# Kernel optimization log

Hardware: AMD Instinct MI355X
Metric: run time of the kernel (lower is better)

## Reference

```python
import jax, jax.numpy as jnp
import numpy as np

B, S, D, H = 2, 2048, 1024, 16
HD = D // H  # head_dim = 64


def setup_inputs() -> dict:
    key = jax.random.key(0)
    ks = jax.random.split(key, 11)
    sc = 1.0 / np.sqrt(D)
    inp = {
        "query": jax.random.normal(ks[0], (B, S, D), jnp.float32),
        "key_": jax.random.normal(ks[1], (B, S, D), jnp.float32),
        "value": jax.random.normal(ks[2], (B, S, D), jnp.float32),
        "Wq": jax.random.normal(ks[3], (D, D), jnp.float32) * sc,
        "bq": jnp.zeros((D,), jnp.float32),
        "Wk": jax.random.normal(ks[4], (D, D), jnp.float32) * sc,
        "bk": jnp.zeros((D,), jnp.float32),
        "Wv": jax.random.normal(ks[5], (D, D), jnp.float32) * sc,
        "bv": jnp.zeros((D,), jnp.float32),
        "Wo": jax.random.normal(ks[6], (D, D), jnp.float32) * sc,
        "bo": jnp.zeros((D,), jnp.float32),
    }
    return inp


def _split_heads(x):
    # [B,S,D] -> [B,H,S,HD]
    return x.reshape(B, -1, H, HD).transpose(0, 2, 1, 3)


def reference(query, key_, value, Wq, bq, Wk, bk, Wv, bv, Wo, bo):
    q = _split_heads(query @ Wq.T + bq)
    k = _split_heads(key_ @ Wk.T + bk)
    v = _split_heads(value @ Wv.T + bv)
    scores = jnp.einsum("bhqd,bhkd->bhqk", q, k) / jnp.sqrt(jnp.float32(HD))
    attn = jax.nn.softmax(scores, axis=-1)  # dropout is identity in eval
    out = jnp.einsum("bhqk,bhkd->bhqd", attn, v)
    out = out.transpose(0, 2, 1, 3).reshape(B, -1, D)
    return out @ Wo.T + bo
```

## Files before the change

kernel.cpp:

```cpp
#include <hip/hip_runtime.h>
#include <hip/hip_bf16.h>
#include <stdint.h>

#define B_  2
#define S_  2048
#define D_  1024
#define H_  16
#define HD_ 64
#define M_  (B_*S_)

typedef __bf16 bf16x8 __attribute__((ext_vector_type(8)));
typedef float  f32x4  __attribute__((ext_vector_type(4)));
typedef unsigned int u32x4 __attribute__((ext_vector_type(4)));
typedef unsigned int u32x2 __attribute__((ext_vector_type(2)));
typedef unsigned short ushort_t;
typedef ushort_t u16x8 __attribute__((ext_vector_type(8)));

#define LOG2E 1.44269504088896f

#if __has_builtin(__builtin_amdgcn_exp2f)
#define EXP2(x) __builtin_amdgcn_exp2f(x)
#else
#define EXP2(x) exp2f(x)
#endif

__device__ __forceinline__ ushort_t f2bf(float f) {
    return __builtin_bit_cast(ushort_t, (__bf16)f);
}
__device__ __forceinline__ bf16x8 load_frag(const ushort_t* p) {
    u32x4 r = *reinterpret_cast<const u32x4*>(p);
    return __builtin_bit_cast(bf16x8, r);
}
__device__ __forceinline__ bf16x8 lds_frag(const ushort_t* p) {
    u32x4 r = *reinterpret_cast<const u32x4*>(p);
    return __builtin_bit_cast(bf16x8, r);
}
__device__ __forceinline__ void gld_lds16(const ushort_t* g, ushort_t* l) {
    __builtin_amdgcn_global_load_lds(
        (const __attribute__((address_space(1))) void*)g,
        (__attribute__((address_space(3))) void*)l, 16, 0, 0);
}

__device__ __forceinline__ void cvt_body(const float* __restrict__ in,
                                         ushort_t* __restrict__ out, int i) {
    f32x4 v0 = *reinterpret_cast<const f32x4*>(in + i);
    f32x4 v1 = *reinterpret_cast<const f32x4*>(in + i + 4);
    u16x8 o;
#pragma unroll
    for (int j = 0; j < 4; ++j) { o[j] = f2bf(v0[j]); o[4 + j] = f2bf(v1[j]); }
    *reinterpret_cast<u16x8*>(out + i) = o;
}

__global__ __launch_bounds__(256) void cvt_all_kernel(
    const float* q, const float* k, const float* v,
    const float* fwq, const float* fwk, const float* fwv, const float* fwo,
    ushort_t* oq, ushort_t* ok, ushort_t* ov,
    ushort_t* owq, ushort_t* owk, ushort_t* owv, ushort_t* owo)
{
    const size_t T = (size_t)M_ * D_;
    const size_t U = (size_t)D_ * D_;
    const size_t idx = ((size_t)blockIdx.x * 256 + threadIdx.x) * 8;
    const float* in; ushort_t* out; size_t off;
    if (idx < 3 * T) {
        const size_t w = idx >> 22; off = idx & (T - 1);
        in  = (w == 0) ? q  : (w == 1) ? k  : v;
        out = (w == 0) ? oq : (w == 1) ? ok : ov;
    } else {
        const size_t r = idx - 3 * T;
        const size_t w = r >> 20; off = r & (U - 1);
        in  = (w == 0) ? fwq : (w == 1) ? fwk : (w == 2) ? fwv : fwo;
        out = (w == 0) ? owq : (w == 1) ? owk : (w == 2) ? owv : owo;
    }
    cvt_body(in, out, (int)off);
}

__device__ __forceinline__ void gemm_body(const ushort_t* __restrict__ X,
                                          const ushort_t* __restrict__ W,
                                          const float* __restrict__ bias,
                                          void* __restrict__ out, int mode)
{
    __shared__ ushort_t lA[3][128 * 32];
    __shared__ ushort_t lB[3][128 * 32];

    const int tid  = threadIdx.x;
    const int lane = tid & 63;
    const int wv   = tid >> 6;
    const int m0   = blockIdx.x * 128;
    const int n0   = blockIdx.y * 128;
    const int wr   = (wv >> 1) * 64;
    const int wc   = (wv & 1) * 64;
    const int l15  = lane & 15;
    const int lg   = lane >> 4;

    f32x4 acc[4][4];
#pragma unroll
    for (int i = 0; i < 4; ++i)
#pragma unroll
        for (int j = 0; j < 4; ++j) acc[i][j] = (f32x4){0.f, 0.f, 0.f, 0.f};

    const int srow = lane >> 2;
    const int sk   = (lane & 3) * 8;
    const int c0   = wv * 2, c1 = wv * 2 + 1;
    const size_t arow0 = (size_t)(m0 + c0 * 16 + srow) * D_ + sk;
    const size_t arow1 = (size_t)(m0 + c1 * 16 + srow) * D_ + sk;
    const size_t brow0 = (size_t)(n0 + c0 * 16 + srow) * D_ + sk;
    const size_t brow1 = (size_t)(n0 + c1 * 16 + srow) * D_ + sk;

    auto stage = [&](int ktile, int bufi) {
        const int k0 = ktile * 32;
        gld_lds16(X + arow0 + k0, &lA[bufi][c0 * 512]);
        gld_lds16(X + arow1 + k0, &lA[bufi][c1 * 512]);
        gld_lds16(W + brow0 + k0, &lB[bufi][c0 * 512]);
        gld_lds16(W + brow1 + k0, &lB[bufi][c1 * 512]);
    };

    const int NKT = D_ / 32;
    stage(0, 0);
    stage(1, 1);

    int cur = 0;
    for (int kt = 0; kt < NKT; ++kt) {
        __builtin_amdgcn_s_barrier();
        if (kt + 2 < NKT) {
            int nxt = cur + 2; if (nxt >= 3) nxt -= 3;
            stage(kt + 2, nxt);
            asm volatile("s_waitcnt vmcnt(8)" ::: "memory");
        } else if (kt + 2 == NKT) {
            asm volatile("s_waitcnt vmcnt(4)" ::: "memory");
        } else {
            asm volatile("s_waitcnt vmcnt(0)" ::: "memory");
        }
        __builtin_amdgcn_s_barrier();
        __builtin_amdgcn_sched_barrier(0);

        bf16x8 a[4], b[4];
#pragma unroll
        for (int i = 0; i < 4; ++i)
            a[i] = lds_frag(&lA[cur][(wr + i * 16 + l15) * 32 + lg * 8]);
#pragma unroll
        for (int j = 0; j < 4; ++j)
            b[j] = lds_frag(&lB[cur][(wc + j * 16 + l15) * 32 + lg * 8]);
#pragma unroll
        for (int i = 0; i < 4; ++i)
#pragma unroll
            for (int j = 0; j < 4; ++j)
                acc[i][j] = __builtin_amdgcn_mfma_f32_16x16x32_bf16(a[i], b[j], acc[i][j], 0, 0, 0);

        cur = (cur == 2) ? 0 : cur + 1;
    }

#pragma unroll
    for (int i = 0; i < 4; ++i) {
#pragma unroll
        for (int j = 0; j < 4; ++j) {
            const int gcol = n0 + wc + j * 16 + l15;
            const float bv = bias[gcol];
#pragma unroll
            for (int r = 0; r < 4; ++r) {
                const int grow = m0 + wr + i * 16 + lg * 4 + r;
                float v = acc[i][j][r] + bv;
                if (mode == 0) v *= 0.125f * LOG2E;
                if (mode == 3) {
                    ((float*)out)[(size_t)grow * D_ + gcol] = v;
                } else {
                    const int b = grow >> 11, s = grow & (S_ - 1);
                    const int h = gcol >> 6,  hd = gcol & 63;
                    size_t addr;
                    if (mode == 2) addr = ((size_t)(b * H_ + h) * HD_ + hd) * S_ + s;
                    else           addr = ((size_t)(b * H_ + h) * S_ + s) * HD_ + hd;
                    ((ushort_t*)out)[addr] = f2bf(v);
                }
            }
        }
    }
}

__global__ __launch_bounds__(256) void qkv_kernel(
    const ushort_t* q_in, const ushort_t* k_in, const ushort_t* v_in,
    const ushort_t* Wq, const ushort_t* Wk, const ushort_t* Wv,
    const float* bq, const float* bk, const float* bv,
    ushort_t* qo, ushort_t* ko, ushort_t* vo)
{
    const int z = blockIdx.z;
    const ushort_t* X  = (z == 0) ? q_in : (z == 1) ? k_in : v_in;
    const ushort_t* W  = (z == 0) ? Wq   : (z == 1) ? Wk   : Wv;
    const float*    bs = (z == 0) ? bq   : (z == 1) ? bk   : bv;
    ushort_t*       o  = (z == 0) ? qo   : (z == 1) ? ko   : vo;
    gemm_body(X, W, bs, o, (z == 2) ? 2 : z);
}

__global__ __launch_bounds__(256) void oproj_kernel(
    const ushort_t* X, const ushort_t* W, const float* bias, float* out)
{
    gemm_body(X, W, bias, out, 3);
}

#define PST2 40
#define KVB 64
#define NT  (S_ / KVB)
#define SM_K0 0
#define SM_K1 4096
#define SM_V0 8192
#define SM_V1 12288
#define SM_P  16384
#define SM_TOT (16384 + 8 * 32 * PST2)

__global__ __launch_bounds__(512, 4) void attn_kernel(
    const ushort_t* __restrict__ Q, const ushort_t* __restrict__ K,
    const ushort_t* __restrict__ VT, ushort_t* __restrict__ O)
{
    __shared__ ushort_t smem[SM_TOT];

    const int lane = threadIdx.x & 63;
    const int wv   = threadIdx.x >> 6;
    const int wq   = wv & 3;
    const int wkv  = wv >> 2;
    const int bh   = blockIdx.x;
    const int qb   = blockIdx.y;
    const int qbase = qb * 128 + wq * 32;
    const int l15  = lane & 15;
    const int lg   = lane >> 4;

    const ushort_t* Qp = Q  + (size_t)bh * S_ * HD_;
    const ushort_t* Kp = K  + (size_t)bh * S_ * HD_;
    const ushort_t* Vp = VT + (size_t)bh * HD_ * S_;

    const int kr = threadIdx.x >> 3;
    const int kc = ((threadIdx.x & 7) ^ (kr & 7)) * 8;
    const int koff = threadIdx.x * 8;

    auto stage = [&](int tile, ushort_t* kdst, ushort_t* vdst) {
        gld_lds16(Kp + (size_t)(tile * KVB + kr) * HD_ + kc, kdst + koff);
        gld_lds16(Vp + (size_t)kr * S_ + tile * KVB + kc,    vdst + koff);
    };

    int offk[2][2];
#pragma unroll
    for (int j = 0; j < 2; ++j)
#pragma unroll
        for (int c = 0; c < 2; ++c)
            offk[j][c] = (wkv * 32 + j * 16 + l15) * 64 +
                         ((c * 32 + lg * 8) ^ ((l15 & 7) << 3));
    int offv[4];
#pragma unroll
    for (int dt = 0; dt < 4; ++dt)
        offv[dt] = (dt * 16 + l15) * 64 +
                   ((wkv * 32 + lg * 8) ^ ((l15 & 7) << 3));

    bf16x8 aq[2][2];
#pragma unroll
    for (int qh = 0; qh < 2; ++qh)
#pragma unroll
        for (int c = 0; c < 2; ++c)
            aq[c][qh] = load_frag(Qp + (size_t)(qbase + qh * 16 + l15) * HD_ + c * 32 + lg * 8);

    f32x4 accO[4][2];
#pragma unroll
    for (int dt = 0; dt < 4; ++dt)
#pragma unroll
        for (int qh = 0; qh < 2; ++qh) accO[dt][qh] = (f32x4){0.f, 0.f, 0.f, 0.f};
    float lrun0 = 0.f, lrun1 = 0.f;

    ushort_t* pbuf = &smem[SM_P + wv * 32 * PST2];

    stage(0, &smem[SM_K0], &smem[SM_V0]);

    for (int t = 0; t < NT; ++t) {
        const int cur = t & 1;
        const ushort_t* kb = cur ? &smem[SM_K1] : &smem[SM_K0];
        const ushort_t* vb = cur ? &smem[SM_V1] : &smem[SM_V0];

        __builtin_amdgcn_s_barrier();
        if (t + 1 < NT) {
            stage(t + 1, cur ? &smem[SM_K0] : &smem[SM_K1],
                          cur ? &smem[SM_V0] : &smem[SM_V1]);
            asm volatile("s_waitcnt vmcnt(2)" ::: "memory");
        } else {
            asm volatile("s_waitcnt vmcnt(0)" ::: "memory");
        }
        __builtin_amdgcn_s_barrier();
        __builtin_amdgcn_sched_barrier(0);

        f32x4 st[2][2];
#pragma unroll
        for (int j = 0; j < 2; ++j)
#pragma unroll
            for (int qh = 0; qh < 2; ++qh) st[j][qh] = (f32x4){0.f, 0.f, 0.f, 0.f};
        __builtin_amdgcn_s_setprio(1);
#pragma unroll
        for (int j = 0; j < 2; ++j) {
            bf16x8 k0 = lds_frag(&kb[offk[j][0]]);
            bf16x8 k1 = lds_frag(&kb[offk[j][1]]);
            st[j][0] = __builtin_amdgcn_mfma_f32_16x16x32_bf16(k0, aq[0][0], st[j][0], 0, 0, 0);
            st[j][0] = __builtin_amdgcn_mfma_f32_16x16x32_bf16(k1, aq[1][0], st[j][0], 0, 0, 0);
            st[j][1] = __builtin_amdgcn_mfma_f32_16x16x32_bf16(k0, aq[0][1], st[j][1], 0, 0, 0);
            st[j][1] = __builtin_amdgcn_mfma_f32_16x16x32_bf16(k1, aq[1][1], st[j][1], 0, 0, 0);
        }
        __builtin_amdgcn_s_setprio(0);

#pragma unroll
        for (int qh = 0; qh < 2; ++qh) {
            float p[2][4];
#pragma unroll
            for (int j = 0; j < 2; ++j)
#pragma unroll
                for (int r = 0; r < 4; ++r)
                    p[j][r] = EXP2(st[j][qh][r]);
#pragma unroll
            for (int j = 0; j < 2; ++j) {
                u32x2 w;
                w[0] = (unsigned)f2bf(p[j][0]) | ((unsigned)f2bf(p[j][1]) << 16);
                w[1] = (unsigned)f2bf(p[j][2]) | ((unsigned)f2bf(p[j][3]) << 16);
                *reinterpret_cast<u32x2*>(
                    &pbuf[(qh * 16 + l15) * PST2 + j * 16 + lg * 4]) = w;
            }
            float s0 = (p[0][0] + p[0][1]) + (p[0][2] + p[0][3]);
            float s1 = (p[1][0] + p[1][1]) + (p[1][2] + p[1][3]);
            if (qh == 0) lrun0 += s0 + s1;
            else         lrun1 += s0 + s1;
        }

        bf16x8 ap[2];
#pragma unroll
        for (int qh = 0; qh < 2; ++qh)
            ap[qh] = lds_frag(&pbuf[(qh * 16 + l15) * PST2 + lg * 8]);

        __builtin_amdgcn_s_setprio(1);
#pragma unroll
        for (int dt = 0; dt < 4; ++dt) {
            bf16x8 vf = lds_frag(&vb[offv[dt]]);
            accO[dt][0] = __builtin_amdgcn_mfma_f32_16x16x32_bf16(vf, ap[0], accO[dt][0], 0, 0, 0);
            accO[dt][1] = __builtin_amdgcn_mfma_f32_16x16x32_bf16(vf, ap[1], accO[dt][1], 0, 0, 0);
        }
        __builtin_amdgcn_s_setprio(0);
    }

    lrun0 += __shfl_xor(lrun0, 16);
    lrun0 += __shfl_xor(lrun0, 32);
    lrun1 += __shfl_xor(lrun1, 16);
    lrun1 += __shfl_xor(lrun1, 32);

    __syncthreads();
    float* cbuf = (float*)smem;

    if (wkv == 1) {
#pragma unroll
        for (int qh = 0; qh < 2; ++qh) {
            const int rowq = (wq * 2 + qh) * 16 + l15;
#pragma unroll
            for (int dt = 0; dt < 4; ++dt)
                *reinterpret_cast<f32x4*>(&cbuf[rowq * 68 + dt * 16 + lg * 4]) = accO[dt][qh];
        }
        if (lane < 16) {
            cbuf[128 * 68 + (wq * 2 + 0) * 16 + lane] = lrun0;
            cbuf[128 * 68 + (wq * 2 + 1) * 16 + lane] = lrun1;
        }
    }
    __syncthreads();

    if (wkv == 0) {
        const int b = bh >> 4, h = bh & 15;
#pragma unroll
        for (int qh = 0; qh < 2; ++qh) {
            const int rowq = (wq * 2 + qh) * 16 + l15;
            const float lsum = (qh == 0 ? lrun0 : lrun1) +
                               cbuf[128 * 68 + rowq - l15 + l15];
            const float inv = 1.0f / (lsum);
            const size_t rowbase =
                (size_t)(b * S_ + qbase + qh * 16 + l15) * D_ + h * 64;
#pragma unroll
            for (int dt = 0; dt < 4; ++dt) {
                f32x4 part = *reinterpret_cast<f32x4*>(&cbuf[rowq * 68 + dt * 16 + lg * 4]);
                f32x4 tot  = accO[dt][qh] + part;
                u32x2 w;
                w[0] = (unsigned)f2bf(tot[0] * inv) | ((unsigned)f2bf(tot[1] * inv) << 16);
                w[1] = (unsigned)f2bf(tot[2] * inv) | ((unsigned)f2bf(tot[3] * inv) << 16);
                *reinterpret_cast<u32x2*>(&O[rowbase + dt * 16 + lg * 4]) = w;
            }
        }
    }
}

extern "C" void kernel_launch(void* const* d_in, const int* in_sizes, int n_in,
                              void* d_out, int out_size, void* d_ws, size_t ws_size,
                              hipStream_t stream)
{
    const float* query = (const float*)d_in[0];
    const float* key_  = (const float*)d_in[1];
    const float* value = (const float*)d_in[2];
    const float* Wq    = (const float*)d_in[3];
    const float* bq    = (const float*)d_in[4];
    const float* Wk    = (const float*)d_in[5];
    const float* bk    = (const float*)d_in[6];
    const float* Wv    = (const float*)d_in[7];
    const float* bv    = (const float*)d_in[8];
    const float* Wo    = (const float*)d_in[9];
    const float* bo    = (const float*)d_in[10];

    ushort_t* ws   = (ushort_t*)d_ws;
    const size_t T = (size_t)M_ * D_;
    const size_t U = (size_t)D_ * D_;
    ushort_t* xq  = ws;
    ushort_t* xk  = xq + T;
    ushort_t* xv  = xk + T;
    ushort_t* wq  = xv + T;
    ushort_t* wk  = wq + U;
    ushort_t* wv  = wk + U;
    ushort_t* wo  = wv + U;
    ushort_t* qws  = wo + U;
    ushort_t* kws  = qws + T;
    ushort_t* vtws = kws + T;
    ushort_t* aows = vtws + T;

    const int cvt_blocks = (int)((3 * T + 4 * U) / (256 * 8));
    cvt_all_kernel<<<cvt_blocks, 256, 0, stream>>>(
        query, key_, value, Wq, Wk, Wv, Wo,
        xq, xk, xv, wq, wk, wv, wo);

    qkv_kernel<<<dim3(32, 8, 3), 256, 0, stream>>>(
        xq, xk, xv, wq, wk, wv, bq, bk, bv, qws, kws, vtws);

    attn_kernel<<<dim3(32, 16), 512, 0, stream>>>(qws, kws, vtws, aows);

    oproj_kernel<<<dim3(32, 8, 1), 256, 0, stream>>>(
        aows, wo, bo, (float*)d_out);
}
```

Before: 127.1 us.

## Software-pipeline attention loop so QK^T of next tile overlaps PV of previous

```diff
diff --git a/kernel.cpp b/kernel.cpp
--- a/kernel.cpp
+++ b/kernel.cpp
@@ -202,8 +202,9 @@
 #define SM_K1 4096
 #define SM_V0 8192
 #define SM_V1 12288
-#define SM_P  16384
-#define SM_TOT (16384 + 8 * 32 * PST2)
+#define SM_P0 16384
+#define SM_P1 26624
+#define SM_TOT 36864
 
 __global__ __launch_bounds__(512, 4) void attn_kernel(
     const ushort_t* __restrict__ Q, const ushort_t* __restrict__ K,
@@ -229,9 +230,11 @@
     const int kc = ((threadIdx.x & 7) ^ (kr & 7)) * 8;
     const int koff = threadIdx.x * 8;
 
-    auto stage = [&](int tile, ushort_t* kdst, ushort_t* vdst) {
+    auto stageK = [&](int tile, ushort_t* kdst) {
         gld_lds16(Kp + (size_t)(tile * KVB + kr) * HD_ + kc, kdst + koff);
-        gld_lds16(Vp + (size_t)kr * S_ + tile * KVB + kc,    vdst + koff);
+    };
+    auto stageV = [&](int tile, ushort_t* vdst) {
+        gld_lds16(Vp + (size_t)kr * S_ + tile * KVB + kc, vdst + koff);
     };
 
     int offk[2][2];
@@ -261,26 +264,44 @@
         for (int qh = 0; qh < 2; ++qh) accO[dt][qh] = (f32x4){0.f, 0.f, 0.f, 0.f};
     float lrun0 = 0.f, lrun1 = 0.f;
 
-    ushort_t* pbuf = &smem[SM_P + wv * 32 * PST2];
-
-    stage(0, &smem[SM_K0], &smem[SM_V0]);
-
-    for (int t = 0; t < NT; ++t) {
-        const int cur = t & 1;
-        const ushort_t* kb = cur ? &smem[SM_K1] : &smem[SM_K0];
-        const ushort_t* vb = cur ? &smem[SM_V1] : &smem[SM_V0];
-
-        __builtin_amdgcn_s_barrier();
-        if (t + 1 < NT) {
-            stage(t + 1, cur ? &smem[SM_K0] : &smem[SM_K1],
-                          cur ? &smem[SM_V0] : &smem[SM_V1]);
-            asm volatile("s_waitcnt vmcnt(2)" ::: "memory");
-        } else {
-            asm volatile("s_waitcnt vmcnt(0)" ::: "memory");
-        }
+    ushort_t* pA = &smem[SM_P0 + wv * 32 * PST2];
+    ushort_t* pB = &smem[SM_P1 + wv * 32 * PST2];
+
+    auto softmax_pack = [&](f32x4 st[2][2], ushort_t* pw) {
+#pragma unroll
+        for (int qh = 0; qh < 2; ++qh) {
+            float p[2][4];
+#pragma unroll
+            for (int j = 0; j < 2; ++j)
+#pragma unroll
+                for (int r = 0; r < 4; ++r)
+                    p[j][r] = EXP2(st[j][qh][r]);
+#pragma unroll
+            for (int j = 0; j < 2; ++j) {
+                u32x2 w;
+                w[0] = (unsigned)f2bf(p[j][0]) | ((unsigned)f2bf(p[j][1]) << 16);
+                w[1] = (unsigned)f2bf(p[j][2]) | ((unsigned)f2bf(p[j][3]) << 16);
+                *reinterpret_cast<u32x2*>(
+                    &pw[(qh * 16 + l15) * PST2 + j * 16 + lg * 4]) = w;
+            }
+            float s0 = (p[0][0] + p[0][1]) + (p[0][2] + p[0][3]);
+            float s1 = (p[1][0] + p[1][1]) + (p[1][2] + p[1][3]);
+            if (qh == 0) lrun0 += s0 + s1;
+            else         lrun1 += s0 + s1;
+        }
+    };
+
+    stageK(0, &smem[SM_K0]);
+
+    {
+        __builtin_amdgcn_s_barrier();
+        stageK(1, &smem[SM_K1]);
+        stageV(0, &smem[SM_V0]);
+        asm volatile("s_waitcnt vmcnt(2)" ::: "memory");
         __builtin_amdgcn_s_barrier();
         __builtin_amdgcn_sched_barrier(0);
 
+        const ushort_t* kb = &smem[SM_K0];
         f32x4 st[2][2];
 #pragma unroll
         for (int j = 0; j < 2; ++j)
@@ -297,42 +318,70 @@
             st[j][1] = __builtin_amdgcn_mfma_f32_16x16x32_bf16(k1, aq[1][1], st[j][1], 0, 0, 0);
         }
         __builtin_amdgcn_s_setprio(0);
-
-#pragma unroll
-        for (int qh = 0; qh < 2; ++qh) {
-            float p[2][4];
-#pragma unroll
-            for (int j = 0; j < 2; ++j)
-#pragma unroll
-                for (int r = 0; r < 4; ++r)
-                    p[j][r] = EXP2(st[j][qh][r]);
-#pragma unroll
-            for (int j = 0; j < 2; ++j) {
-                u32x2 w;
-                w[0] = (unsigned)f2bf(p[j][0]) | ((unsigned)f2bf(p[j][1]) << 16);
-                w[1] = (unsigned)f2bf(p[j][2]) | ((unsigned)f2bf(p[j][3]) << 16);
-                *reinterpret_cast<u32x2*>(
-                    &pbuf[(qh * 16 + l15) * PST2 + j * 16 + lg * 4]) = w;
-            }
-            float s0 = (p[0][0] + p[0][1]) + (p[0][2] + p[0][3]);
-            float s1 = (p[1][0] + p[1][1]) + (p[1][2] + p[1][3]);
-            if (qh == 0) lrun0 += s0 + s1;
-            else         lrun1 += s0 + s1;
-        }
+        softmax_pack(st, pA);
+    }
+
+    for (int t = 1; t < NT; ++t) {
+        const int cur = t & 1;
+        const ushort_t* kb  = cur ? &smem[SM_K1] : &smem[SM_K0];
+        const ushort_t* vbp = cur ? &smem[SM_V0] : &smem[SM_V1];
+        ushort_t* pw = cur ? pB : pA;
+        const ushort_t* pr = cur ? pA : pB;
+
+        __builtin_amdgcn_s_barrier();
+        stageK(t + 1, cur ? &smem[SM_K0] : &smem[SM_K1]);
+        stageV(t, cur ? &smem[SM_V1] : &smem[SM_V0]);
+        asm volatile("s_waitcnt vmcnt(2)" ::: "memory");
+        __builtin_amdgcn_s_barrier();
+        __builtin_amdgcn_sched_barrier(0);
 
         bf16x8 ap[2];
 #pragma unroll
         for (int qh = 0; qh < 2; ++qh)
-            ap[qh] = lds_frag(&pbuf[(qh * 16 + l15) * PST2 + lg * 8]);
+            ap[qh] = lds_frag(&pr[(qh * 16 + l15) * PST2 + lg * 8]);
+
+        f32x4 st[2][2];
+#pragma unroll
+        for (int j = 0; j < 2; ++j)
+#pragma unroll
+            for (int qh = 0; qh < 2; ++qh) st[j][qh] = (f32x4){0.f, 0.f, 0.f, 0.f};
 
         __builtin_amdgcn_s_setprio(1);
 #pragma unroll
+        for (int j = 0; j < 2; ++j) {
+            bf16x8 k0 = lds_frag(&kb[offk[j][0]]);
+            bf16x8 k1 = lds_frag(&kb[offk[j][1]]);
+            st[j][0] = __builtin_amdgcn_mfma_f32_16x16x32_bf16(k0, aq[0][0], st[j][0], 0, 0, 0);
+            st[j][0] = __builtin_amdgcn_mfma_f32_16x16x32_bf16(k1, aq[1][0], st[j][0], 0, 0, 0);
+            st[j][1] = __builtin_amdgcn_mfma_f32_16x16x32_bf16(k0, aq[0][1], st[j][1], 0, 0, 0);
+            st[j][1] = __builtin_amdgcn_mfma_f32_16x16x32_bf16(k1, aq[1][1], st[j][1], 0, 0, 0);
+        }
+#pragma unroll
         for (int dt = 0; dt < 4; ++dt) {
-            bf16x8 vf = lds_frag(&vb[offv[dt]]);
+            bf16x8 vf = lds_frag(&vbp[offv[dt]]);
             accO[dt][0] = __builtin_amdgcn_mfma_f32_16x16x32_bf16(vf, ap[0], accO[dt][0], 0, 0, 0);
             accO[dt][1] = __builtin_amdgcn_mfma_f32_16x16x32_bf16(vf, ap[1], accO[dt][1], 0, 0, 0);
         }
         __builtin_amdgcn_s_setprio(0);
+
+        softmax_pack(st, pw);
+    }
+
+    {
+        asm volatile("s_waitcnt vmcnt(0)" ::: "memory");
+        __builtin_amdgcn_s_barrier();
+        const ushort_t* vbp = ((NT - 1) & 1) ? &smem[SM_V1] : &smem[SM_V0];
+        const ushort_t* pr  = ((NT - 1) & 1) ? pB : pA;
+        bf16x8 ap[2];
+#pragma unroll
+        for (int qh = 0; qh < 2; ++qh)
+            ap[qh] = lds_frag(&pr[(qh * 16 + l15) * PST2 + lg * 8]);
+#pragma unroll
+        for (int dt = 0; dt < 4; ++dt) {
+            bf16x8 vf = lds_frag(&vbp[offv[dt]]);
+            accO[dt][0] = __builtin_amdgcn_mfma_f32_16x16x32_bf16(vf, ap[0], accO[dt][0], 0, 0, 0);
+            accO[dt][1] = __builtin_amdgcn_mfma_f32_16x16x32_bf16(vf, ap[1], accO[dt][1], 0, 0, 0);
+        }
     }
 
     lrun0 += __shfl_xor(lrun0, 16);
@@ -363,9 +412,8 @@
 #pragma unroll
         for (int qh = 0; qh < 2; ++qh) {
             const int rowq = (wq * 2 + qh) * 16 + l15;
-            const float lsum = (qh == 0 ? lrun0 : lrun1) +
-                               cbuf[128 * 68 + rowq - l15 + l15];
-            const float inv = 1.0f / (lsum);
+            const float lsum = (qh == 0 ? lrun0 : lrun1) + cbuf[128 * 68 + rowq];
+            const float inv = 1.0f / lsum;
             const size_t rowbase =
                 (size_t)(b * S_ + qbase + qh * 16 + l15) * D_ + h * 64;
 #pragma unroll
```

After: 127.4 us. About the same (+0.2%).

## Keep softmax probabilities in registers via 16x16x16 MFMA; double-buffer GEMM

Applied to the files above, without the earlier changes.

```diff
diff --git a/kernel.cpp b/kernel.cpp
--- a/kernel.cpp
+++ b/kernel.cpp
@@ -10,6 +10,8 @@
 #define M_  (B_*S_)
 
 typedef __bf16 bf16x8 __attribute__((ext_vector_type(8)));
+typedef __bf16 bf16x4 __attribute__((ext_vector_type(4)));
+typedef short  s16x4  __attribute__((ext_vector_type(4)));
 typedef float  f32x4  __attribute__((ext_vector_type(4)));
 typedef unsigned int u32x4 __attribute__((ext_vector_type(4)));
 typedef unsigned int u32x2 __attribute__((ext_vector_type(2)));
@@ -35,10 +37,28 @@
     u32x4 r = *reinterpret_cast<const u32x4*>(p);
     return __builtin_bit_cast(bf16x8, r);
 }
+__device__ __forceinline__ bf16x4 lds_frag4(const ushort_t* p) {
+    u32x2 r = *reinterpret_cast<const u32x2*>(p);
+    return __builtin_bit_cast(bf16x4, r);
+}
 __device__ __forceinline__ void gld_lds16(const ushort_t* g, ushort_t* l) {
     __builtin_amdgcn_global_load_lds(
         (const __attribute__((address_space(1))) void*)g,
         (__attribute__((address_space(3))) void*)l, 16, 0, 0);
+}
+
+__device__ __forceinline__ f32x4 mfma16_bf16(bf16x4 a, bf16x4 b, f32x4 c) {
+#if __has_builtin(__builtin_amdgcn_mfma_f32_16x16x16_bf16)
+    return __builtin_amdgcn_mfma_f32_16x16x16_bf16(a, b, c, 0, 0, 0);
+#elif __has_builtin(__builtin_amdgcn_mfma_f32_16x16x16bf16_1k)
+    return __builtin_amdgcn_mfma_f32_16x16x16bf16_1k(
+        __builtin_bit_cast(s16x4, a), __builtin_bit_cast(s16x4, b), c, 0, 0, 0);
+#else
+    f32x4 d;
+    asm("v_mfma_f32_16x16x16_bf16 %0, %1, %2, %3"
+        : "=v"(d) : "v"(a), "v"(b), "v"(c));
+    return d;
+#endif
 }
 
 __device__ __forceinline__ void cvt_body(const float* __restrict__ in,
@@ -79,8 +99,8 @@
                                           const float* __restrict__ bias,
                                           void* __restrict__ out, int mode)
 {
-    __shared__ ushort_t lA[3][128 * 32];
-    __shared__ ushort_t lB[3][128 * 32];
+    __shared__ ushort_t lA[2][128 * 32];
+    __shared__ ushort_t lB[2][128 * 32];
 
     const int tid  = threadIdx.x;
     const int lane = tid & 63;
@@ -106,32 +126,26 @@
     const size_t brow0 = (size_t)(n0 + c0 * 16 + srow) * D_ + sk;
     const size_t brow1 = (size_t)(n0 + c1 * 16 + srow) * D_ + sk;
 
-    auto stage = [&](int ktile, int bufi) {
-        const int k0 = ktile * 32;
-        gld_lds16(X + arow0 + k0, &lA[bufi][c0 * 512]);
-        gld_lds16(X + arow1 + k0, &lA[bufi][c1 * 512]);
-        gld_lds16(W + brow0 + k0, &lB[bufi][c0 * 512]);
-        gld_lds16(W + brow1 + k0, &lB[bufi][c1 * 512]);
-    };
+    gld_lds16(X + arow0, &lA[0][c0 * 512]);
+    gld_lds16(X + arow1, &lA[0][c1 * 512]);
+    gld_lds16(W + brow0, &lB[0][c0 * 512]);
+    gld_lds16(W + brow1, &lB[0][c1 * 512]);
 
     const int NKT = D_ / 32;
-    stage(0, 0);
-    stage(1, 1);
-
-    int cur = 0;
     for (int kt = 0; kt < NKT; ++kt) {
+        const int cur = kt & 1;
         __builtin_amdgcn_s_barrier();
-        if (kt + 2 < NKT) {
-            int nxt = cur + 2; if (nxt >= 3) nxt -= 3;
-            stage(kt + 2, nxt);
-            asm volatile("s_waitcnt vmcnt(8)" ::: "memory");
-        } else if (kt + 2 == NKT) {
+        if (kt + 1 < NKT) {
+            const int k0 = (kt + 1) * 32;
+            gld_lds16(X + arow0 + k0, &lA[cur ^ 1][c0 * 512]);
+            gld_lds16(X + arow1 + k0, &lA[cur ^ 1][c1 * 512]);
+            gld_lds16(W + brow0 + k0, &lB[cur ^ 1][c0 * 512]);
+            gld_lds16(W + brow1 + k0, &lB[cur ^ 1][c1 * 512]);
             asm volatile("s_waitcnt vmcnt(4)" ::: "memory");
         } else {
             asm volatile("s_waitcnt vmcnt(0)" ::: "memory");
         }
         __builtin_amdgcn_s_barrier();
-        __builtin_amdgcn_sched_barrier(0);
 
         bf16x8 a[4], b[4];
 #pragma unroll
@@ -145,8 +159,6 @@
 #pragma unroll
             for (int j = 0; j < 4; ++j)
                 acc[i][j] = __builtin_amdgcn_mfma_f32_16x16x32_bf16(a[i], b[j], acc[i][j], 0, 0, 0);
-
-        cur = (cur == 2) ? 0 : cur + 1;
     }
 
 #pragma unroll
@@ -195,15 +207,13 @@
     gemm_body(X, W, bias, out, 3);
 }
 
-#define PST2 40
 #define KVB 64
 #define NT  (S_ / KVB)
 #define SM_K0 0
 #define SM_K1 4096
 #define SM_V0 8192
 #define SM_V1 12288
-#define SM_P  16384
-#define SM_TOT (16384 + 8 * 32 * PST2)
+#define SM_TOT 17920
 
 __global__ __launch_bounds__(512, 4) void attn_kernel(
     const ushort_t* __restrict__ Q, const ushort_t* __restrict__ K,
@@ -241,11 +251,14 @@
         for (int c = 0; c < 2; ++c)
             offk[j][c] = (wkv * 32 + j * 16 + l15) * 64 +
                          ((c * 32 + lg * 8) ^ ((l15 & 7) << 3));
-    int offv[4];
+    int offv[4][2];
 #pragma unroll
     for (int dt = 0; dt < 4; ++dt)
-        offv[dt] = (dt * 16 + l15) * 64 +
-                   ((wkv * 32 + lg * 8) ^ ((l15 & 7) << 3));
+#pragma unroll
+        for (int j = 0; j < 2; ++j)
+            offv[dt][j] = (dt * 16 + l15) * 64 +
+                          (((wkv * 4 + j * 2 + (lg >> 1)) ^ (l15 & 7)) << 3) +
+                          (lg & 1) * 4;
 
     bf16x8 aq[2][2];
 #pragma unroll
@@ -260,8 +273,6 @@
 #pragma unroll
         for (int qh = 0; qh < 2; ++qh) accO[dt][qh] = (f32x4){0.f, 0.f, 0.f, 0.f};
     float lrun0 = 0.f, lrun1 = 0.f;
-
-    ushort_t* pbuf = &smem[SM_P + wv * 32 * PST2];
 
     stage(0, &smem[SM_K0], &smem[SM_V0]);
 
@@ -298,39 +309,33 @@
         }
         __builtin_amdgcn_s_setprio(0);
 
+        bf16x4 pb[2][2];
 #pragma unroll
         for (int qh = 0; qh < 2; ++qh) {
-            float p[2][4];
-#pragma unroll
-            for (int j = 0; j < 2; ++j)
-#pragma unroll
-                for (int r = 0; r < 4; ++r)
-                    p[j][r] = EXP2(st[j][qh][r]);
 #pragma unroll
             for (int j = 0; j < 2; ++j) {
+                float p0 = EXP2(st[j][qh][0]);
+                float p1 = EXP2(st[j][qh][1]);
+                float p2 = EXP2(st[j][qh][2]);
+                float p3 = EXP2(st[j][qh][3]);
                 u32x2 w;
-                w[0] = (unsigned)f2bf(p[j][0]) | ((unsigned)f2bf(p[j][1]) << 16);
-                w[1] = (unsigned)f2bf(p[j][2]) | ((unsigned)f2bf(p[j][3]) << 16);
-                *reinterpret_cast<u32x2*>(
-                    &pbuf[(qh * 16 + l15) * PST2 + j * 16 + lg * 4]) = w;
+                w[0] = (unsigned)f2bf(p0) | ((unsigned)f2bf(p1) << 16);
+                w[1] = (unsigned)f2bf(p2) | ((unsigned)f2bf(p3) << 16);
+                pb[j][qh] = __builtin_bit_cast(bf16x4, w);
+                const float s = (p0 + p1) + (p2 + p3);
+                if (qh == 0) lrun0 += s; else lrun1 += s;
             }
-            float s0 = (p[0][0] + p[0][1]) + (p[0][2] + p[0][3]);
-            float s1 = (p[1][0] + p[1][1]) + (p[1][2] + p[1][3]);
-            if (qh == 0) lrun0 += s0 + s1;
-            else         lrun1 += s0 + s1;
-        }
-
-        bf16x8 ap[2];
-#pragma unroll
-        for (int qh = 0; qh < 2; ++qh)
-            ap[qh] = lds_frag(&pbuf[(qh * 16 + l15) * PST2 + lg * 8]);
+        }
 
         __builtin_amdgcn_s_setprio(1);
 #pragma unroll
         for (int dt = 0; dt < 4; ++dt) {
-            bf16x8 vf = lds_frag(&vb[offv[dt]]);
-            accO[dt][0] = __builtin_amdgcn_mfma_f32_16x16x32_bf16(vf, ap[0], accO[dt][0], 0, 0, 0);
-            accO[dt][1] = __builtin_amdgcn_mfma_f32_16x16x32_bf16(vf, ap[1], accO[dt][1], 0, 0, 0);
+#pragma unroll
+            for (int j = 0; j < 2; ++j) {
+                bf16x4 vf = lds_frag4(&vb[offv[dt][j]]);
+                accO[dt][0] = mfma16_bf16(vf, pb[j][0], accO[dt][0]);
+                accO[dt][1] = mfma16_bf16(vf, pb[j][1], accO[dt][1]);
+            }
         }
         __builtin_amdgcn_s_setprio(0);
     }
@@ -363,9 +368,8 @@
 #pragma unroll
         for (int qh = 0; qh < 2; ++qh) {
             const int rowq = (wq * 2 + qh) * 16 + l15;
-            const float lsum = (qh == 0 ? lrun0 : lrun1) +
-                               cbuf[128 * 68 + rowq - l15 + l15];
-            const float inv = 1.0f / (lsum);
+            const float lsum = (qh == 0 ? lrun0 : lrun1) + cbuf[128 * 68 + rowq];
+            const float inv = 1.0f / lsum;
             const size_t rowbase =
                 (size_t)(b * S_ + qbase + qh * 16 + l15) * D_ + h * 64;
 #pragma unroll
```

New measurement: 133.4 us. 5.0% more time.
